# Optimization experiments

Hardware: AMD Instinct MI355X
Metric: run time of the kernel (lower is better)

The kernel has to match this reference:

```python
import jax, jax.numpy as jnp
import numpy as np

H = 32                         # LSTM_size
K = 3                          # k_value
NK, ND, NU = 4 * K + 2, K, K   # kernel / down / up step counts
T = NK + ND + NU
NEG = -1e9                     # finite mask value (avoids -inf NaNs)


def setup_inputs() -> dict:
    key = jax.random.key(0)
    ks = jax.random.split(key, 12)
    u = lambda k, s: jax.random.uniform(k, s, jnp.float32, -0.1, 0.1)
    return {
        "w_ih": u(ks[0], (4 * H, H)),
        "w_hh": u(ks[1], (4 * H, H)),
        "b_ih": u(ks[2], (4 * H,)),
        "b_hh": u(ks[3], (4 * H,)),
        "g_emb": u(ks[4], (1, H)),
        "emb_kernel": u(ks[5], (8, H)),
        "emb_down": u(ks[6], (3, H)),
        "emb_up": u(ks[7], (3, H)),
        "w_kernel": u(ks[8], (8, H)),
        "w_down": u(ks[9], (3, H)),
        "w_up": u(ks[10], (3, H)),
        "uniform_noise": jax.random.uniform(ks[11], (T, 8), jnp.float32),
    }


def _pad8(w):
    # zero-pad a [n<=8, H] table/head to [8, H]
    return jnp.pad(w, ((0, 8 - w.shape[0]), (0, 0)))


def _forward(w_ih, w_hh, b_ih, b_hh, g_emb, emb_kernel, emb_down, emb_up,
             w_kernel, w_down, w_up, uniform_noise):
    # Per-step projection heads [T, 8, H]; 3-class heads zero-padded to 8 and masked.
    proj = jnp.concatenate([
        jnp.broadcast_to(w_kernel, (NK, 8, H)),
        jnp.broadcast_to(_pad8(w_down), (ND, 8, H)),
        jnp.broadcast_to(_pad8(w_up), (NU, 8, H)),
    ])
    # Per-step embedding table used to embed the sampled action for the NEXT step.
    emb = jnp.concatenate([
        jnp.broadcast_to(emb_kernel, (NK, 8, H)),
        jnp.broadcast_to(_pad8(emb_down), (ND, 8, H)),
        jnp.broadcast_to(_pad8(emb_up), (NU, 8, H)),
    ])
    m3 = jnp.array([1, 1, 1, 0, 0, 0, 0, 0], dtype=bool)
    mask = jnp.concatenate([
        jnp.ones((NK, 8), dtype=bool),
        jnp.broadcast_to(m3, (ND, 8)),
        jnp.broadcast_to(m3, (NU, 8)),
    ])
    # Gumbel-max categorical sampling noise.
    gumbel = -jnp.log(-jnp.log(uniform_noise * (1.0 - 1e-6) + 1e-7))

    def step(carry, xs):
        h, c, x = carry                                   # h, c, x: [H]
        Wp, Et, msk, g = xs
        # Torch LSTM cell: gates = W_ih x + b_ih + W_hh h + b_hh, order i,f,g,o
        gates = w_ih @ x + b_ih + w_hh @ h + b_hh         # [4H]
        i, f, gg, o = jnp.split(gates, 4)
        c = jax.nn.sigmoid(f) * c + jax.nn.sigmoid(i) * jnp.tanh(gg)
        h = jax.nn.sigmoid(o) * jnp.tanh(c)
        logits = jnp.where(msk, Wp @ h, NEG)              # [8]
        logp = jax.nn.log_softmax(logits)
        s = jnp.argmax(logits + g)                        # Categorical sample
        p = jnp.where(msk, jnp.exp(logp), 0.0)
        ent = -jnp.sum(p * jnp.where(msk, logp, 0.0))
        return (h, c, Et[s]), (logp[s], ent, s)

    init = (jnp.zeros((H,), jnp.float32), jnp.zeros((H,), jnp.float32), g_emb[0])
    _, (lps, ents, samples) = jax.lax.scan(step, init, (proj, emb, mask, gumbel))
    # stats = [sample_log_prob, sample_entropy]
    return jnp.stack([jnp.sum(lps), jnp.sum(ents)]), samples


def reference(w_ih, w_hh, b_ih, b_hh, g_emb, emb_kernel, emb_down, emb_up,
              w_kernel, w_down, w_up, uniform_noise):
    return _forward(w_ih, w_hh, b_ih, b_hh, g_emb, emb_kernel, emb_down, emb_up,
                    w_kernel, w_down, w_up, uniform_noise)
```

## Files before the change

kernel.cpp:

```cpp
#include <hip/hip_runtime.h>

#define HH 32
#define TT 20

typedef float v2f __attribute__((ext_vector_type(2)));

#define LOG2E  1.4426950408889634f
#define LN2    0.6931471805599453f

__device__ __forceinline__ float fsig(float x) {
    return __builtin_amdgcn_rcpf(1.0f + __builtin_amdgcn_exp2f(-x * LOG2E));
}
__device__ __forceinline__ float ftanh(float x) {
    return 1.0f - 2.0f * __builtin_amdgcn_rcpf(1.0f + __builtin_amdgcn_exp2f(x * (2.0f * LOG2E)));
}

__global__ __launch_bounds__(64, 1) void controller_kernel(
    const float* __restrict__ w_ih,
    const float* __restrict__ w_hh,
    const float* __restrict__ b_ih,
    const float* __restrict__ b_hh,
    const float* __restrict__ g_emb,
    const float* __restrict__ emb_kernel,
    const float* __restrict__ emb_down,
    const float* __restrict__ emb_up,
    const float* __restrict__ w_kernel,
    const float* __restrict__ w_down,
    const float* __restrict__ w_up,
    const float* __restrict__ noise,
    float* __restrict__ out)
{
    const int t   = threadIdx.x;
    const int q   = t & 31;
    const int cls = t & 7;

    __shared__ __align__(16) float emb_s[15 * 32];
    __shared__ __align__(16) float Gv[15 * 32 * 4];
    __shared__ __align__(16) float h_s[32];
    __shared__ __align__(16) float gum_s[TT * 8];
    __shared__ __align__(16) float head_pre[2 * 64 * 4];

    for (int i = t; i < 15 * 32; i += 64) {
        const int r = i >> 5, j = i & 31;
        float v;
        if (r < 8)       v = emb_kernel[i];
        else if (r < 11) v = emb_down[i - 8 * 32];
        else if (r < 14) v = emb_up[i - 11 * 32];
        else             v = g_emb[j];
        emb_s[i] = v;
    }
    for (int i = t; i < TT * 8; i += 64) {
        const float u = noise[i];
        gum_s[i] = -logf(-logf(u * (1.0f - 1e-6f) + 1e-7f));
    }
#pragma unroll
    for (int bi = 0; bi < 2; ++bi) {
        float4 v = make_float4(0.f, 0.f, 0.f, 0.f);
        if (cls < 3) {
            const float* W = (bi == 0) ? w_down : w_up;
            v = *(const float4*)(W + cls * 32 + (t >> 3) * 4);
        }
        *(float4*)(head_pre + (bi * 64 + t) * 4) = v;
    }

    float bias[4];
#pragma unroll
    for (int g = 0; g < 4; ++g) bias[g] = b_ih[q + 32 * g] + b_hh[q + 32 * g];

    {
        v2f wih[64];
#pragma unroll
        for (int g = 0; g < 4; ++g) {
            const float4* p = (const float4*)(w_ih + (q + 32 * g) * HH);
#pragma unroll
            for (int k8 = 0; k8 < 8; ++k8) {
                const float4 a = p[k8];
                wih[g * 16 + 2 * k8]     = (v2f){a.x, a.y};
                wih[g * 16 + 2 * k8 + 1] = (v2f){a.z, a.w};
            }
        }
        __syncthreads();
        const int e0 = (t < 32) ? 0 : 8;
        const int e1 = (t < 32) ? 8 : 15;
        for (int e = e0; e < e1; ++e) {
            const float4* ep = (const float4*)(emb_s + e * 32);
            v2f g0 = {0.f,0.f}, g1 = {0.f,0.f}, g2 = {0.f,0.f}, g3 = {0.f,0.f};
#pragma unroll
            for (int k8 = 0; k8 < 8; ++k8) {
                const float4 a = ep[k8];
                const v2f x0 = {a.x, a.y}, x1 = {a.z, a.w};
                g0 += wih[2*k8]    * x0;  g0 += wih[2*k8+1]    * x1;
                g1 += wih[16+2*k8] * x0;  g1 += wih[16+2*k8+1] * x1;
                g2 += wih[32+2*k8] * x0;  g2 += wih[32+2*k8+1] * x1;
                g3 += wih[48+2*k8] * x0;  g3 += wih[48+2*k8+1] * x1;
            }
            *(float4*)(Gv + (e * 32 + q) * 4) =
                make_float4(bias[0] + g0.x + g0.y, bias[1] + g1.x + g1.y,
                            bias[2] + g2.x + g2.y, bias[3] + g3.x + g3.y);
        }
    }
    __syncthreads();
    __builtin_amdgcn_sched_barrier(0);

    v2f whh[64];
#pragma unroll
    for (int g = 0; g < 4; ++g) {
        const float4* p = (const float4*)(w_hh + (q + 32 * g) * HH);
#pragma unroll
        for (int k8 = 0; k8 < 8; ++k8) {
            const float4 a = p[k8];
            whh[g * 16 + 2 * k8]     = (v2f){a.x, a.y};
            whh[g * 16 + 2 * k8 + 1] = (v2f){a.z, a.w};
        }
    }
    v2f hk[16];
#pragma unroll
    for (int k8 = 0; k8 < 8; ++k8) {
        const float4 a = ((const float4*)(w_kernel + cls * 32))[k8];
        hk[2*k8] = (v2f){a.x, a.y}; hk[2*k8+1] = (v2f){a.z, a.w};
    }

    v2f hreg[16];
#pragma unroll
    for (int k = 0; k < 16; ++k) hreg[k] = (v2f){0.f, 0.f};
    float  c_reg = 0.0f;
    float4 G4 = *(const float4*)(Gv + (14 * 32 + q) * 4);
    float  lp_sum = 0.0f, ent_sum = 0.0f;

    for (int step = 0; step < TT; ++step) {
        v2f ai = {0.f,0.f}, af = {0.f,0.f}, ag = {0.f,0.f}, ao = {0.f,0.f};
#pragma unroll
        for (int k = 0; k < 16; ++k) {
            ai += whh[k]      * hreg[k];
            af += whh[16 + k] * hreg[k];
            ag += whh[32 + k] * hreg[k];
            ao += whh[48 + k] * hreg[k];
        }
        const float gi_ = G4.x + ai.x + ai.y;
        const float gf_ = G4.y + af.x + af.y;
        const float gg_ = G4.z + ag.x + ag.y;
        const float go_ = G4.w + ao.x + ao.y;

        const float ig = fsig(gi_), fg = fsig(gf_), gv = ftanh(gg_), og = fsig(go_);
        c_reg = fg * c_reg + ig * gv;
        const float hn = og * ftanh(c_reg);
        if (t < 32) h_s[t] = hn;
        __syncthreads();

#pragma unroll
        for (int k8 = 0; k8 < 8; ++k8) {
            const float4 hv = ((const float4*)h_s)[k8];
            hreg[2*k8] = (v2f){hv.x, hv.y}; hreg[2*k8+1] = (v2f){hv.z, hv.w};
        }

        float l;
        if (step < 14) {
            v2f s0 = {0.f,0.f}, s1 = {0.f,0.f};
#pragma unroll
            for (int k = 0; k < 16; k += 2) { s0 += hk[k]*hreg[k]; s1 += hk[k+1]*hreg[k+1]; }
            l = (s0.x + s0.y) + (s1.x + s1.y);
        } else {
            const int bi = (step < 17) ? 0 : 1;
            const float4 hp = *(const float4*)(head_pre + (bi * 64 + t) * 4);
            const float4 hv = ((const float4*)h_s)[t >> 3];
            float p = hp.x*hv.x + hp.y*hv.y + hp.z*hv.z + hp.w*hv.w;
            p += __shfl_xor(p, 8);
            p += __shfl_xor(p, 16);
            p += __shfl_xor(p, 32);
            l = (cls < 3) ? p : -1e9f;
        }

        float lv[8];
#pragma unroll
        for (int k = 0; k < 8; ++k) lv[k] = __shfl(l, k);

        float S = 0.0f, Tm = 0.0f;
#pragma unroll
        for (int k = 0; k < 8; ++k) {
            const float e = __builtin_amdgcn_exp2f(lv[k] * LOG2E);
            S += e; Tm += e * lv[k];
        }
        const float4 gA = ((const float4*)(gum_s + step * 8))[0];
        const float4 gB = ((const float4*)(gum_s + step * 8))[1];
        const float v0 = lv[0]+gA.x, v1 = lv[1]+gA.y, v2 = lv[2]+gA.z, v3 = lv[3]+gA.w;
        const float v4 = lv[4]+gB.x, v5 = lv[5]+gB.y, v6 = lv[6]+gB.z, v7 = lv[7]+gB.w;
        const bool ta = v1 > v0;  const float va = ta?v1:v0;  const int ia = ta?1:0;  const float la = ta?lv[1]:lv[0];
        const bool tb = v3 > v2;  const float vb = tb?v3:v2;  const int ib = tb?3:2;  const float lb = tb?lv[3]:lv[2];
        const bool tc = v5 > v4;  const float vc = tc?v5:v4;  const int ic = tc?5:4;  const float lc = tc?lv[5]:lv[4];
        const bool td = v7 > v6;  const float vd = td?v7:v6;  const int id_= td?7:6;  const float ld = td?lv[7]:lv[6];
        const bool tab = vb > va; const float vab = tab?vb:va; const int iab = tab?ib:ia; const float lab = tab?lb:la;
        const bool tcd = vd > vc; const float vcd = tcd?vd:vc; const int icd = tcd?id_:ic; const float lcd = tcd?ld:lc;
        const bool tf  = vcd > vab;
        const int   idx = tf ? icd : iab;
        const float bl  = tf ? lcd : lab;

        const float lse = __builtin_amdgcn_logf(S) * LN2;
        lp_sum  += bl - lse;
        ent_sum += lse - Tm * __builtin_amdgcn_rcpf(S);
        if (t == 0) out[2 + step] = (float)idx;

        const int base = (step < 14) ? 0 : ((step < 17) ? 8 : 11);
        G4 = *(const float4*)(Gv + ((base + idx) * 32 + q) * 4);
    }

    if (t == 0) {
        out[0] = lp_sum;
        out[1] = ent_sum;
    }
}

extern "C" void kernel_launch(void* const* d_in, const int* in_sizes, int n_in,
                              void* d_out, int out_size, void* d_ws, size_t ws_size,
                              hipStream_t stream) {
    (void)in_sizes; (void)n_in; (void)out_size; (void)d_ws; (void)ws_size;
    const float* w_ih       = (const float*)d_in[0];
    const float* w_hh       = (const float*)d_in[1];
    const float* b_ih       = (const float*)d_in[2];
    const float* b_hh       = (const float*)d_in[3];
    const float* g_emb      = (const float*)d_in[4];
    const float* emb_kernel = (const float*)d_in[5];
    const float* emb_down   = (const float*)d_in[6];
    const float* emb_up     = (const float*)d_in[7];
    const float* w_kernel   = (const float*)d_in[8];
    const float* w_down     = (const float*)d_in[9];
    const float* w_up       = (const float*)d_in[10];
    const float* noise      = (const float*)d_in[11];
    float* out = (float*)d_out;

    hipLaunchKernelGGL(controller_kernel, dim3(1), dim3(64), 0, stream,
                       w_ih, w_hh, b_ih, b_hh, g_emb, emb_kernel, emb_down,
                       emb_up, w_kernel, w_down, w_up, noise, out);
}
```

Baseline: 94.17 us.

## Broadcast hidden state via readlane and overlap recurrent matvec with sampling

The hidden state is now broadcast to all lanes with readlane from registers instead of being written to LDS and read back after a barrier, which removes the per-step __syncthreads. The loop is restructured so the W_hh·h matvec for the next step is computed alongside the logits before the sample is known, and only the input-gate lookup waits on the sampled index. The down and up heads are staged into LDS and swapped into the head registers at the phase boundaries, so every step uses one uniform dot-product path. The cost is 32 scalar readlanes per step plus higher VGPR pressure from holding whh as 128 scalar floats.

```diff
diff --git a/kernel.cpp b/kernel.cpp
--- a/kernel.cpp
+++ b/kernel.cpp
@@ -8,6 +8,9 @@
 #define LOG2E  1.4426950408889634f
 #define LN2    0.6931471805599453f
 
+__device__ __forceinline__ float rl(float v, int k) {
+    return __int_as_float(__builtin_amdgcn_readlane(__float_as_int(v), k));
+}
 __device__ __forceinline__ float fsig(float x) {
     return __builtin_amdgcn_rcpf(1.0f + __builtin_amdgcn_exp2f(-x * LOG2E));
 }
@@ -36,9 +39,8 @@
 
     __shared__ __align__(16) float emb_s[15 * 32];
     __shared__ __align__(16) float Gv[15 * 32 * 4];
-    __shared__ __align__(16) float h_s[32];
     __shared__ __align__(16) float gum_s[TT * 8];
-    __shared__ __align__(16) float head_pre[2 * 64 * 4];
+    __shared__ __align__(16) float head_s[2 * 8 * 32];
 
     for (int i = t; i < 15 * 32; i += 64) {
         const int r = i >> 5, j = i & 31;
@@ -53,14 +55,9 @@
         const float u = noise[i];
         gum_s[i] = -logf(-logf(u * (1.0f - 1e-6f) + 1e-7f));
     }
-#pragma unroll
-    for (int bi = 0; bi < 2; ++bi) {
-        float4 v = make_float4(0.f, 0.f, 0.f, 0.f);
-        if (cls < 3) {
-            const float* W = (bi == 0) ? w_down : w_up;
-            v = *(const float4*)(W + cls * 32 + (t >> 3) * 4);
-        }
-        *(float4*)(head_pre + (bi * 64 + t) * 4) = v;
+    for (int i = t; i < 2 * 8 * 32; i += 64) {
+        const int bi = i >> 8, r = (i >> 5) & 7, j = i & 31;
+        head_s[i] = (r < 3) ? (bi ? w_up[r * 32 + j] : w_down[r * 32 + j]) : 0.0f;
     }
 
     float bias[4];
@@ -102,84 +99,64 @@
     __syncthreads();
     __builtin_amdgcn_sched_barrier(0);
 
-    v2f whh[64];
+    float whh[128];
 #pragma unroll
     for (int g = 0; g < 4; ++g) {
         const float4* p = (const float4*)(w_hh + (q + 32 * g) * HH);
 #pragma unroll
         for (int k8 = 0; k8 < 8; ++k8) {
             const float4 a = p[k8];
-            whh[g * 16 + 2 * k8]     = (v2f){a.x, a.y};
-            whh[g * 16 + 2 * k8 + 1] = (v2f){a.z, a.w};
-        }
-    }
-    v2f hk[16];
+            whh[g*32 + 4*k8 + 0] = a.x; whh[g*32 + 4*k8 + 1] = a.y;
+            whh[g*32 + 4*k8 + 2] = a.z; whh[g*32 + 4*k8 + 3] = a.w;
+        }
+    }
+    float hc[32];
 #pragma unroll
     for (int k8 = 0; k8 < 8; ++k8) {
         const float4 a = ((const float4*)(w_kernel + cls * 32))[k8];
-        hk[2*k8] = (v2f){a.x, a.y}; hk[2*k8+1] = (v2f){a.z, a.w};
-    }
-
-    v2f hreg[16];
-#pragma unroll
-    for (int k = 0; k < 16; ++k) hreg[k] = (v2f){0.f, 0.f};
-    float  c_reg = 0.0f;
-    float4 G4 = *(const float4*)(Gv + (14 * 32 + q) * 4);
-    float  lp_sum = 0.0f, ent_sum = 0.0f;
+        hc[4*k8+0] = a.x; hc[4*k8+1] = a.y; hc[4*k8+2] = a.z; hc[4*k8+3] = a.w;
+    }
+
+    float c_reg, hn;
+    {
+        const float4 G0 = *(const float4*)(Gv + (14 * 32 + q) * 4);
+        const float ig = fsig(G0.x), fg0 = fsig(G0.y), gv = ftanh(G0.z), og = fsig(G0.w);
+        (void)fg0;
+        c_reg = ig * gv;
+        hn    = og * ftanh(c_reg);
+    }
+    float lp_sum = 0.0f, ent_sum = 0.0f;
 
     for (int step = 0; step < TT; ++step) {
-        v2f ai = {0.f,0.f}, af = {0.f,0.f}, ag = {0.f,0.f}, ao = {0.f,0.f};
-#pragma unroll
-        for (int k = 0; k < 16; ++k) {
-            ai += whh[k]      * hreg[k];
-            af += whh[16 + k] * hreg[k];
-            ag += whh[32 + k] * hreg[k];
-            ao += whh[48 + k] * hreg[k];
-        }
-        const float gi_ = G4.x + ai.x + ai.y;
-        const float gf_ = G4.y + af.x + af.y;
-        const float gg_ = G4.z + ag.x + ag.y;
-        const float go_ = G4.w + ao.x + ao.y;
-
-        const float ig = fsig(gi_), fg = fsig(gf_), gv = ftanh(gg_), og = fsig(go_);
-        c_reg = fg * c_reg + ig * gv;
-        const float hn = og * ftanh(c_reg);
-        if (t < 32) h_s[t] = hn;
-        __syncthreads();
-
-#pragma unroll
-        for (int k8 = 0; k8 < 8; ++k8) {
-            const float4 hv = ((const float4*)h_s)[k8];
-            hreg[2*k8] = (v2f){hv.x, hv.y}; hreg[2*k8+1] = (v2f){hv.z, hv.w};
-        }
-
-        float l;
-        if (step < 14) {
-            v2f s0 = {0.f,0.f}, s1 = {0.f,0.f};
-#pragma unroll
-            for (int k = 0; k < 16; k += 2) { s0 += hk[k]*hreg[k]; s1 += hk[k+1]*hreg[k+1]; }
-            l = (s0.x + s0.y) + (s1.x + s1.y);
-        } else {
-            const int bi = (step < 17) ? 0 : 1;
-            const float4 hp = *(const float4*)(head_pre + (bi * 64 + t) * 4);
-            const float4 hv = ((const float4*)h_s)[t >> 3];
-            float p = hp.x*hv.x + hp.y*hv.y + hp.z*hv.z + hp.w*hv.w;
-            p += __shfl_xor(p, 8);
-            p += __shfl_xor(p, 16);
-            p += __shfl_xor(p, 32);
-            l = (cls < 3) ? p : -1e9f;
+        float sh[32];
+#pragma unroll
+        for (int k = 0; k < 32; ++k) sh[k] = rl(hn, k);
+
+        float l0 = 0.f, l1 = 0.f, l2 = 0.f, l3 = 0.f;
+#pragma unroll
+        for (int k = 0; k < 32; k += 4) {
+            l0 += hc[k]   * sh[k];
+            l1 += hc[k+1] * sh[k+1];
+            l2 += hc[k+2] * sh[k+2];
+            l3 += hc[k+3] * sh[k+3];
+        }
+        const int n = (step < 14) ? 8 : 3;
+        float l = (l0 + l1) + (l2 + l3);
+        l = (cls < n) ? l : -1e9f;
+
+        float Mi = 0.f, Mf = 0.f, Mg = 0.f, Mo = 0.f;
+#pragma unroll
+        for (int k = 0; k < 32; ++k) {
+            Mi += whh[k]      * sh[k];
+            Mf += whh[32 + k] * sh[k];
+            Mg += whh[64 + k] * sh[k];
+            Mo += whh[96 + k] * sh[k];
         }
 
         float lv[8];
 #pragma unroll
-        for (int k = 0; k < 8; ++k) lv[k] = __shfl(l, k);
-
-        float S = 0.0f, Tm = 0.0f;
-#pragma unroll
-        for (int k = 0; k < 8; ++k) {
-            const float e = __builtin_amdgcn_exp2f(lv[k] * LOG2E);
-            S += e; Tm += e * lv[k];
-        }
+        for (int k = 0; k < 8; ++k) lv[k] = rl(l, k);
+
         const float4 gA = ((const float4*)(gum_s + step * 8))[0];
         const float4 gB = ((const float4*)(gum_s + step * 8))[1];
         const float v0 = lv[0]+gA.x, v1 = lv[1]+gA.y, v2 = lv[2]+gA.z, v3 = lv[3]+gA.w;
@@ -194,13 +171,33 @@
         const int   idx = tf ? icd : iab;
         const float bl  = tf ? lcd : lab;
 
+        const int base = (step < 14) ? 0 : ((step < 17) ? 8 : 11);
+        const float4 G4 = *(const float4*)(Gv + ((base + idx) * 32 + q) * 4);
+
+        const float gi_ = G4.x + Mi, gf_ = G4.y + Mf, gg_ = G4.z + Mg, go_ = G4.w + Mo;
+        const float ig = fsig(gi_), fg = fsig(gf_), gv = ftanh(gg_), og = fsig(go_);
+        c_reg = fg * c_reg + ig * gv;
+        hn    = og * ftanh(c_reg);
+
+        float S = 0.0f, Tm = 0.0f;
+#pragma unroll
+        for (int k = 0; k < 8; ++k) {
+            const float e = __builtin_amdgcn_exp2f(lv[k] * LOG2E);
+            S += e; Tm += e * lv[k];
+        }
         const float lse = __builtin_amdgcn_logf(S) * LN2;
         lp_sum  += bl - lse;
         ent_sum += lse - Tm * __builtin_amdgcn_rcpf(S);
         if (t == 0) out[2 + step] = (float)idx;
 
-        const int base = (step < 14) ? 0 : ((step < 17) ? 8 : 11);
-        G4 = *(const float4*)(Gv + ((base + idx) * 32 + q) * 4);
+        if (step == 13 || step == 16) {
+            const float* src = head_s + ((step == 16) ? 8 * 32 : 0) + cls * 32;
+#pragma unroll
+            for (int k8 = 0; k8 < 8; ++k8) {
+                const float4 a = ((const float4*)src)[k8];
+                hc[4*k8+0] = a.x; hc[4*k8+1] = a.y; hc[4*k8+2] = a.z; hc[4*k8+3] = a.w;
+            }
+        }
     }
 
     if (t == 0) {
```

New measurement: 97.42 us. +3.5%, slower.
